# Performance work log

Hardware: AMD Instinct MI355X
Metric: run time of the kernel (lower is better)

The kernel has to match this reference:

```python
import jax, jax.numpy as jnp
import numpy as np
from jax import lax

N = 32768; L = 3000; PER_GRAPH = 64; NUM_GRAPHS = N // PER_GRAPH
DEG = 16; E = N * DEG
HID = 128; OUT3 = 64; NCLS = 2
RED = (L - 100) // 20 + 1   # 146
F_IN = 32 * RED             # 4672
EPS = 1e-5


def setup_inputs() -> dict:
    key = jax.random.key(0)
    ks = jax.random.split(key, 16)
    x = jax.random.normal(ks[0], (N, L), jnp.float32)
    # within-graph random edges: dst stays inside src's graph block
    src = jnp.repeat(jnp.arange(N, dtype=jnp.int32), DEG)
    dst = (src // PER_GRAPH) * PER_GRAPH + jax.random.randint(ks[1], (E,), 0, PER_GRAPH, dtype=jnp.int32)
    edge_index = jnp.stack([src, dst])
    edge_attr = jax.random.uniform(ks[2], (E,), jnp.float32, 0.1, 1.0)
    batch = jnp.repeat(jnp.arange(NUM_GRAPHS, dtype=jnp.int32), PER_GRAPH)
    g = lambda k, sh, fan: jax.random.normal(k, sh, jnp.float32) / np.float32(np.sqrt(fan))
    def bn(k, c):
        k1, k2 = jax.random.split(k)
        return (jnp.ones(c, jnp.float32), jnp.zeros(c, jnp.float32),
                0.1 * jax.random.normal(k1, (c,), jnp.float32),
                jax.random.uniform(k2, (c,), jnp.float32, 0.5, 1.5))
    g1, be1, m1, v1 = bn(ks[7], HID)
    g2, be2, m2, v2 = bn(ks[8], HID)
    g3, be3, m3, v3 = bn(ks[9], OUT3)
    return dict(x=x, edge_index=edge_index, edge_attr=edge_attr, batch=batch,
                conv_w=g(ks[3], (32, 1, 100), 100), conv_b=jnp.zeros(32, jnp.float32),
                W1=g(ks[4], (F_IN, HID), F_IN), b1=jnp.zeros(HID, jnp.float32),
                W2=g(ks[5], (HID, HID), HID), b2=jnp.zeros(HID, jnp.float32),
                W3=g(ks[6], (HID, OUT3), HID), b3=jnp.zeros(OUT3, jnp.float32),
                g1=g1, be1=be1, m1=m1, v1=v1,
                g2=g2, be2=be2, m2=m2, v2=v2,
                g3=g3, be3=be3, m3=m3, v3=v3,
                fc_w=g(ks[10], (OUT3, NCLS), OUT3), fc_b=jnp.zeros(NCLS, jnp.float32))


def _gcn(h, W, b, src, dst, w):
    # PyG GCNConv: linear (no bias) -> sym-normalized weighted aggregation with
    # self-loops (weight 1) -> + bias
    h = h @ W                                               # [N, C]
    deg = jax.ops.segment_sum(w, dst, num_segments=N) + 1.0  # + self-loop
    dinv = jnp.where(deg > 0, lax.rsqrt(deg), 0.0)
    norm = dinv[src] * w * dinv[dst]                         # [E]
    agg = jax.ops.segment_sum(h[src] * norm[:, None], dst, num_segments=N)
    return agg + h * (dinv * dinv)[:, None] + b              # self-loop term


def _bn(x, gamma, beta, mean, var):
    # eval-mode BatchNorm1d with running stats
    return (x - mean) * lax.rsqrt(var + EPS) * gamma + beta


def reference(x, edge_index, edge_attr, batch, conv_w, conv_b, W1, b1, W2, b2, W3, b3,
              g1, be1, m1, v1, g2, be2, m2, v2, g3, be3, m3, v3, fc_w, fc_b):
    src, dst = edge_index[0], edge_index[1]
    # Conv1d feature extractor: [N,1,L] -> [N,32,RED]
    h = lax.conv_general_dilated(x[:, None, :], conv_w, (20,), 'VALID',
                                 dimension_numbers=('NCH', 'OIH', 'NCH'))
    h = jax.nn.relu(h + conv_b[None, :, None]).reshape(N, F_IN)
    h = jax.nn.relu(_bn(_gcn(h, W1, b1, src, dst, edge_attr), g1, be1, m1, v1))
    h = jax.nn.relu(_bn(_gcn(h, W2, b2, src, dst, edge_attr), g2, be2, m2, v2))
    h = jax.nn.relu(_bn(_gcn(h, W3, b3, src, dst, edge_attr), g3, be3, m3, v3))
    # global mean pool over graphs
    sums = jax.ops.segment_sum(h, batch, num_segments=NUM_GRAPHS)
    cnt = jax.ops.segment_sum(jnp.ones((N,), h.dtype), batch, num_segments=NUM_GRAPHS)
    pooled = sums / cnt[:, None]
    return jax.nn.log_softmax(pooled @ fc_w + fc_b, axis=1)
```

## Files before the change

kernel.cpp:

```cpp
#include <hip/hip_runtime.h>
#include <math.h>

typedef float f32x4 __attribute__((ext_vector_type(4)));
typedef short bf16x8 __attribute__((ext_vector_type(8)));
typedef unsigned int u32;
typedef unsigned long long u64;

constexpr int N_NODES = 32768;
constexpr int LEN     = 3000;
constexpr int HID     = 128;
constexpr int OUT3    = 64;
constexpr int E_TOT   = 32768*16;
constexpr int PG      = 64;
constexpr int EPG     = 1024;
constexpr int NG      = 512;
constexpr int NCHUNK  = 25;
constexpr int XS_S    = 260;
constexpr int CBS     = 196;

__device__ __forceinline__ short bf1(float a) {
    unsigned u = __float_as_uint(a);
    return (short)((u + 0x7fff + ((u >> 16) & 1)) >> 16);
}
__device__ __forceinline__ u32 pk2(float lo, float hi) {
    u32 ua = __float_as_uint(lo) + 0x8000u;
    u32 ub = __float_as_uint(hi) + 0x8000u;
    return (ua >> 16) | (ub & 0xffff0000u);
}

__device__ __forceinline__ void bar_lds() {
    asm volatile("s_waitcnt lgkmcnt(0)" ::: "memory");
    __builtin_amdgcn_s_barrier();
}

__global__ void pack_w(const float* __restrict__ cw, short* __restrict__ wPf) {
    int tid = blockIdx.x * 256 + threadIdx.x;
    if (tid >= 512) return;
    int lane = tid & 63, i = tid >> 6;
    int Mt = i >> 2, ks = i & 3;
    int c  = Mt * 16 + (lane & 15);
    int kb = ks * 32 + (lane >> 4) * 8;
    bf16x8 v;
    #pragma unroll
    for (int j = 0; j < 8; j++) {
        int k = kb + j;
        v[j] = (k < 100) ? bf1(cw[c * 100 + k]) : (short)0;
    }
    *(bf16x8*)(wPf + tid * 8) = v;
}

__global__ void pack_w1(const float* __restrict__ W1, short* __restrict__ w1f) {
    int tid = blockIdx.x * 256 + threadIdx.x;
    if (tid >= 76800) return;
    int lane  = tid & 63;
    int rest  = tid >> 6;
    int ks    = rest % 6;
    int rest2 = rest / 6;
    int Nt    = rest2 & 7, chunk = rest2 >> 3;
    int r  = chunk * 6 + ks;
    int n  = Nt * 16 + (lane & 15);
    int cb = (lane >> 4) * 8;
    bf16x8 v;
    #pragma unroll
    for (int j = 0; j < 8; j++) {
        int c = cb + j;
        v[j] = (r < 146) ? bf1(W1[(c * 146 + r) * 128 + n]) : (short)0;
    }
    *(bf16x8*)(w1f + tid * 8) = v;
}

__global__ __launch_bounds__(256, 2) void conv_gemm1_mfma(
    const float* __restrict__ x, const short* __restrict__ wPf,
    const float* __restrict__ cbv, const short* __restrict__ w1f,
    float* __restrict__ z)
{
    __shared__ short xs[64 * XS_S];
    __shared__ short cbuf[64 * CBS];

    const int t     = threadIdx.x;
    const int lane  = t & 63;
    const int wv    = t >> 6;
    const int l15   = lane & 15;
    const int q     = lane >> 4;
    const int n0    = blockIdx.x * 64;
    const int j4    = lane & 3;
    const int nodeS = wv * 16 + (lane >> 2);
    const int nodeC = wv * 16 + l15;

    bf16x8 wA[8];
    #pragma unroll
    for (int i = 0; i < 8; i++)
        wA[i] = *(const bf16x8*)(wPf + (i * 64 + lane) * 8);
    float cbr[8];
    #pragma unroll
    for (int i = 0; i < 8; i++)
        cbr[i] = cbv[(i >> 2) * 16 + q * 4 + (i & 3)];

    f32x4 acc[4][2];
    #pragma unroll
    for (int a = 0; a < 4; a++) { acc[a][0] = (f32x4)0.0f; acc[a][1] = (f32x4)0.0f; }

    const int NtG0 = wv * 2;
    const float* xpS = x + (size_t)(n0 + nodeS) * LEN;
    short* xrow = xs + nodeS * XS_S;

    {
        float4 v[13];
        #pragma unroll
        for (int it = 0; it < 13; it++)
            v[it] = *(const float4*)(xpS + (j4 + 4 * it) * 4);
        #pragma unroll
        for (int it = 0; it < 13; it++) {
            int e = (j4 + 4 * it) * 4;
            *(uint2*)&xrow[e] = make_uint2(pk2(v[it].x, v[it].y), pk2(v[it].z, v[it].w));
        }
    }

    #pragma unroll 1
    for (int c = 0; c < NCHUNK; c++) {
        const int r0 = c * 6;
        const int rcount = (146 - r0 < 6) ? (146 - r0) : 6;

        float4 xn[8];
        if (c < NCHUNK - 1) {
            const int ebase = 120 * c + 200;
            #pragma unroll
            for (int it = 0; it < 8; it++) {
                int e  = ebase + (j4 + 4 * it) * 4;
                int ge = e > 2996 ? 2996 : e;
                xn[it] = *(const float4*)(xpS + ge);
            }
        }
        bf16x8 wB[12];
        #pragma unroll
        for (int u = 0; u < 12; u++)
            wB[u] = *(const bf16x8*)(w1f + ((c * 48 + NtG0 * 6 + u) * 64 + lane) * 8);

        bar_lds();

        const short* xr = xs + nodeC * XS_S;
        #pragma unroll
        for (int rr = 0; rr < 6; rr++) {
            const int eb = 20 * (r0 + rr) + 8 * q;
            f32x4 ca0 = (f32x4)0.0f, ca1 = (f32x4)0.0f;
            #pragma unroll
            for (int ks = 0; ks < 4; ks++) {
                int e0 = eb + 32 * ks;
                bf16x8 bx;
                *(u64*)&bx       = *(const u64*)&xr[e0 & 255];
                *((u64*)&bx + 1) = *(const u64*)&xr[(e0 + 4) & 255];
                ca0 = __builtin_amdgcn_mfma_f32_16x16x32_bf16(wA[ks],     bx, ca0, 0, 0, 0);
                ca1 = __builtin_amdgcn_mfma_f32_16x16x32_bf16(wA[4 + ks], bx, ca1, 0, 0, 0);
            }
            short* cw_ = cbuf + nodeC * CBS + rr * 32 + q * 4;
            if (rr < rcount) {
                u32 p0 = pk2(fmaxf(ca0[0] + cbr[0], 0.f), fmaxf(ca0[1] + cbr[1], 0.f));
                u32 p1 = pk2(fmaxf(ca0[2] + cbr[2], 0.f), fmaxf(ca0[3] + cbr[3], 0.f));
                *(uint2*)cw_ = make_uint2(p0, p1);
                p0 = pk2(fmaxf(ca1[0] + cbr[4], 0.f), fmaxf(ca1[1] + cbr[5], 0.f));
                p1 = pk2(fmaxf(ca1[2] + cbr[6], 0.f), fmaxf(ca1[3] + cbr[7], 0.f));
                *(uint2*)(cw_ + 16) = make_uint2(p0, p1);
            } else {
                *(uint2*)cw_        = make_uint2(0u, 0u);
                *(uint2*)(cw_ + 16) = make_uint2(0u, 0u);
            }
        }

        if (c < NCHUNK - 1) {
            const int ebase = 120 * c + 200;
            #pragma unroll
            for (int it = 0; it < 8; it++) {
                int e = ebase + (j4 + 4 * it) * 4;
                *(uint2*)&xrow[e & 255] = make_uint2(pk2(xn[it].x, xn[it].y), pk2(xn[it].z, xn[it].w));
            }
        }

        bar_lds();

        #pragma unroll
        for (int ks = 0; ks < 6; ks++) {
            bf16x8 af[4];
            #pragma unroll
            for (int mt = 0; mt < 4; mt++) {
                const short* ap = cbuf + (mt * 16 + l15) * CBS + ks * 32 + q * 8;
                *(u64*)&af[mt]       = *(const u64*)ap;
                *((u64*)&af[mt] + 1) = *(const u64*)(ap + 4);
            }
            #pragma unroll
            for (int mt = 0; mt < 4; mt++) {
                acc[mt][0] = __builtin_amdgcn_mfma_f32_16x16x32_bf16(af[mt], wB[ks],     acc[mt][0], 0, 0, 0);
                acc[mt][1] = __builtin_amdgcn_mfma_f32_16x16x32_bf16(af[mt], wB[6 + ks], acc[mt][1], 0, 0, 0);
            }
        }
    }

    #pragma unroll
    for (int mt = 0; mt < 4; mt++)
        #pragma unroll
        for (int nt2 = 0; nt2 < 2; nt2++)
            #pragma unroll
            for (int reg = 0; reg < 4; reg++) {
                int node = n0 + mt * 16 + q * 4 + reg;
                int f    = (NtG0 + nt2) * 16 + l15;
                z[(size_t)node * HID + f] = acc[mt][nt2][reg];
            }
}

__global__ __launch_bounds__(256) void graph_block(
    const float* __restrict__ z, const int* __restrict__ ei,
    const float* __restrict__ ew,
    const float* __restrict__ b1, const float* __restrict__ g1, const float* __restrict__ be1,
    const float* __restrict__ m1, const float* __restrict__ v1,
    const float* __restrict__ W2,
    const float* __restrict__ b2, const float* __restrict__ g2, const float* __restrict__ be2,
    const float* __restrict__ m2, const float* __restrict__ v2,
    const float* __restrict__ W3,
    const float* __restrict__ b3, const float* __restrict__ g3, const float* __restrict__ be3,
    const float* __restrict__ m3, const float* __restrict__ v3,
    const float* __restrict__ fcw, const float* __restrict__ fcb,
    float* __restrict__ out)
{
    __shared__ float At[64 * 68];
    __shared__ float buf[8704];
    __shared__ float dl[64];
    __shared__ float ps4[256];
    __shared__ float pooled[64];

    const int t  = threadIdx.x;
    const int g  = blockIdx.x;
    const int nb = g * PG;

    for (int i = t; i < 64 * 68; i += 256) At[i] = 0.f;
    if (t < 64) dl[t] = 0.f;
    __syncthreads();
    for (int i = t; i < EPG; i += 256) {
        int e = g * EPG + i;
        atomicAdd(&dl[ei[E_TOT + e] - nb], ew[e]);
    }
    __syncthreads();
    if (t < 64) dl[t] = rsqrtf(dl[t] + 1.0f);
    __syncthreads();
    for (int i = t; i < EPG; i += 256) {
        int e = g * EPG + i;
        int s = ei[e] - nb, d = ei[E_TOT + e] - nb;
        atomicAdd(&At[s * 68 + d], dl[s] * ew[e] * dl[d]);
    }
    if (t < 64) atomicAdd(&At[t * 68 + t], dl[t] * dl[t]);
    for (int i = t; i < 64 * HID; i += 256) buf[i] = z[(size_t)nb * HID + i];
    __syncthreads();

    const int f   = t & 127;
    const int ng  = t >> 7;
    const int n0  = ng * 32;
    const int f3  = t & 63;
    const int ng3 = t >> 6;
    const int n03 = ng3 * 16;

    float hreg[32];

#define LAYER128(BB, GG, BE, MM, VV)                                          \
    {                                                                         \
        float sc = GG[f] * rsqrtf(VV[f] + 1e-5f);                             \
        float mu = MM[f], bt = BE[f], bb = BB[f];                             \
        float a[32];                                                          \
        _Pragma("unroll")                                                     \
        for (int i = 0; i < 32; i++) a[i] = 0.f;                              \
        _Pragma("unroll 2")                                                   \
        for (int s = 0; s < 64; s++) {                                        \
            float zv = buf[s * 128 + f];                                      \
            _Pragma("unroll")                                                 \
            for (int qq = 0; qq < 8; qq++) {                                  \
                float4 a4 = *(const float4*)&At[s * 68 + n0 + qq * 4];        \
                a[qq*4+0] += a4.x * zv; a[qq*4+1] += a4.y * zv;               \
                a[qq*4+2] += a4.z * zv; a[qq*4+3] += a4.w * zv;               \
            }                                                                 \
        }                                                                     \
        _Pragma("unroll")                                                     \
        for (int i = 0; i < 32; i++)                                          \
            hreg[i] = fmaxf((a[i] + bb - mu) * sc + bt, 0.f);                 \
    }                                                                         \
    __syncthreads();                                                          \
    _Pragma("unroll")                                                         \
    for (int qq = 0; qq < 8; qq++)                                            \
        *(float4*)&buf[f * 68 + n0 + qq * 4] =                                \
            make_float4(hreg[qq*4], hreg[qq*4+1], hreg[qq*4+2], hreg[qq*4+3]);\
    __syncthreads();

#define GEMM128(WPTR)                                                         \
    {                                                                         \
        float a[32];                                                          \
        _Pragma("unroll")                                                     \
        for (int i = 0; i < 32; i++) a[i] = 0.f;                              \
        _Pragma("unroll 2")                                                   \
        for (int k = 0; k < 128; k++) {                                       \
            float wvv = WPTR[k * 128 + f];                                    \
            _Pragma("unroll")                                                 \
            for (int qq = 0; qq < 8; qq++) {                                  \
                float4 h4 = *(const float4*)&buf[k * 68 + n0 + qq * 4];       \
                a[qq*4+0] += h4.x * wvv; a[qq*4+1] += h4.y * wvv;             \
                a[qq*4+2] += h4.z * wvv; a[qq*4+3] += h4.w * wvv;             \
            }                                                                 \
        }                                                                     \
        __syncthreads();                                                      \
        _Pragma("unroll")                                                     \
        for (int i = 0; i < 32; i++) buf[(n0 + i) * 128 + f] = a[i];          \
        __syncthreads();                                                      \
    }

    LAYER128(b1, g1, be1, m1, v1)
    GEMM128(W2)
    LAYER128(b2, g2, be2, m2, v2)

    {
        float a[16];
        #pragma unroll
        for (int i = 0; i < 16; i++) a[i] = 0.f;
        #pragma unroll 2
        for (int k = 0; k < 128; k++) {
            float wvv = W3[k * 64 + f3];
            #pragma unroll
            for (int qq = 0; qq < 4; qq++) {
                float4 h4 = *(const float4*)&buf[k * 68 + n03 + qq * 4];
                a[qq*4+0] += h4.x * wvv; a[qq*4+1] += h4.y * wvv;
                a[qq*4+2] += h4.z * wvv; a[qq*4+3] += h4.w * wvv;
            }
        }
        __syncthreads();
        #pragma unroll
        for (int i = 0; i < 16; i++) buf[(n03 + i) * 64 + f3] = a[i];
        __syncthreads();
    }

    {
        float sc = g3[f3] * rsqrtf(v3[f3] + 1e-5f);
        float mu = m3[f3], bt = be3[f3], bb = b3[f3];
        float a[16];
        #pragma unroll
        for (int i = 0; i < 16; i++) a[i] = 0.f;
        #pragma unroll 2
        for (int s = 0; s < 64; s++) {
            float zv = buf[s * 64 + f3];
            #pragma unroll
            for (int qq = 0; qq < 4; qq++) {
                float4 a4 = *(const float4*)&At[s * 68 + n03 + qq * 4];
                a[qq*4+0] += a4.x * zv; a[qq*4+1] += a4.y * zv;
                a[qq*4+2] += a4.z * zv; a[qq*4+3] += a4.w * zv;
            }
        }
        float psum = 0.f;
        #pragma unroll
        for (int i = 0; i < 16; i++)
            psum += fmaxf((a[i] + bb - mu) * sc + bt, 0.f);
        ps4[ng3 * 64 + f3] = psum;
    }
    __syncthreads();
    if (t < 64) pooled[t] = (ps4[t] + ps4[64 + t] + ps4[128 + t] + ps4[192 + t]) * (1.f / 64.f);
    __syncthreads();
    if (t == 0) {
        float l0 = fcb[0], l1 = fcb[1];
        for (int ff = 0; ff < 64; ff++) { l0 += pooled[ff] * fcw[ff * 2]; l1 += pooled[ff] * fcw[ff * 2 + 1]; }
        float mx  = fmaxf(l0, l1);
        float lse = mx + logf(expf(l0 - mx) + expf(l1 - mx));
        out[g * 2 + 0] = l0 - lse;
        out[g * 2 + 1] = l1 - lse;
    }
#undef LAYER128
#undef GEMM128
}

extern "C" void kernel_launch(void* const* d_in, const int* in_sizes, int n_in,
                              void* d_out, int out_size, void* d_ws, size_t ws_size,
                              hipStream_t stream) {
    const float* x   = (const float*)d_in[0];
    const int*   ei  = (const int*)  d_in[1];
    const float* ew  = (const float*)d_in[2];
    const float* cw  = (const float*)d_in[4];
    const float* cb  = (const float*)d_in[5];
    const float* W1  = (const float*)d_in[6];
    const float* b1  = (const float*)d_in[7];
    const float* W2  = (const float*)d_in[8];
    const float* b2  = (const float*)d_in[9];
    const float* W3  = (const float*)d_in[10];
    const float* b3  = (const float*)d_in[11];
    const float* g1  = (const float*)d_in[12];
    const float* be1 = (const float*)d_in[13];
    const float* m1  = (const float*)d_in[14];
    const float* v1  = (const float*)d_in[15];
    const float* g2  = (const float*)d_in[16];
    const float* be2 = (const float*)d_in[17];
    const float* m2  = (const float*)d_in[18];
    const float* v2  = (const float*)d_in[19];
    const float* g3  = (const float*)d_in[20];
    const float* be3 = (const float*)d_in[21];
    const float* m3  = (const float*)d_in[22];
    const float* v3  = (const float*)d_in[23];
    const float* fcw = (const float*)d_in[24];
    const float* fcb = (const float*)d_in[25];
    float* out = (float*)d_out;

    float* z   = (float*)d_ws;
    short* wPf = (short*)((char*)d_ws + 16777216);
    short* w1f = (short*)((char*)d_ws + 16785408);

    pack_w  <<<2,   256, 0, stream>>>(cw, wPf);
    pack_w1 <<<300, 256, 0, stream>>>(W1, w1f);
    conv_gemm1_mfma<<<NG, 256, 0, stream>>>(x, wPf, cb, w1f, z);
    graph_block<<<NG, 256, 0, stream>>>(z, ei, ew,
        b1, g1, be1, m1, v1, W2,
        b2, g2, be2, m2, v2, W3,
        b3, g3, be3, m3, v3, fcw, fcb, out);
}
```

Measured before the change: 679.6 us.

## Fuse conv/GEMM1 kernel with per-graph GCN kernel via shared-memory handoff

Merges the conv+first-linear MFMA kernel and the per-graph GCN/BN/pool kernel into one kernel. Each block handles one graph and writes its z tile into shared memory instead of global memory. A single aliased shared buffer is reused across both phases. This removes the 16 MB z round trip and one launch, but the graph phase now runs under the (256,2) launch bound and the larger shared footprint, which may limit registers and occupancy.

```diff
diff --git a/kernel.cpp b/kernel.cpp
--- a/kernel.cpp
+++ b/kernel.cpp
@@ -69,20 +69,37 @@
     *(bf16x8*)(w1f + tid * 8) = v;
 }
 
-__global__ __launch_bounds__(256, 2) void conv_gemm1_mfma(
+__global__ __launch_bounds__(256, 2) void fused_all(
     const float* __restrict__ x, const short* __restrict__ wPf,
     const float* __restrict__ cbv, const short* __restrict__ w1f,
-    float* __restrict__ z)
+    const int* __restrict__ ei, const float* __restrict__ ew,
+    const float* __restrict__ b1, const float* __restrict__ g1, const float* __restrict__ be1,
+    const float* __restrict__ m1, const float* __restrict__ v1,
+    const float* __restrict__ W2,
+    const float* __restrict__ b2, const float* __restrict__ g2, const float* __restrict__ be2,
+    const float* __restrict__ m2, const float* __restrict__ v2,
+    const float* __restrict__ W3,
+    const float* __restrict__ b3, const float* __restrict__ g3, const float* __restrict__ be3,
+    const float* __restrict__ m3, const float* __restrict__ v3,
+    const float* __restrict__ fcw, const float* __restrict__ fcb,
+    float* __restrict__ out)
 {
-    __shared__ short xs[64 * XS_S];
-    __shared__ short cbuf[64 * CBS];
+    __shared__ __align__(16) char smraw[58368];
+    short* xs   = (short*)smraw;
+    short* cbuf = (short*)(smraw + 64 * XS_S * 2);
+    float* At     = (float*)smraw;
+    float* buf    = (float*)(smraw + 17408);
+    float* dl     = (float*)(smraw + 52224);
+    float* ps4    = (float*)(smraw + 52480);
+    float* pooled = (float*)(smraw + 53504);
 
     const int t     = threadIdx.x;
     const int lane  = t & 63;
     const int wv    = t >> 6;
     const int l15   = lane & 15;
     const int q     = lane >> 4;
-    const int n0    = blockIdx.x * 64;
+    const int g     = blockIdx.x;
+    const int nbase = g * 64;
     const int j4    = lane & 3;
     const int nodeS = wv * 16 + (lane >> 2);
     const int nodeC = wv * 16 + l15;
@@ -101,7 +118,7 @@
     for (int a = 0; a < 4; a++) { acc[a][0] = (f32x4)0.0f; acc[a][1] = (f32x4)0.0f; }
 
     const int NtG0 = wv * 2;
-    const float* xpS = x + (size_t)(n0 + nodeS) * LEN;
+    const float* xpS = x + (size_t)(nbase + nodeS) * LEN;
     short* xrow = xs + nodeS * XS_S;
 
     {
@@ -194,44 +211,22 @@
         }
     }
 
-    #pragma unroll
-    for (int mt = 0; mt < 4; mt++)
-        #pragma unroll
-        for (int nt2 = 0; nt2 < 2; nt2++)
-            #pragma unroll
-            for (int reg = 0; reg < 4; reg++) {
-                int node = n0 + mt * 16 + q * 4 + reg;
-                int f    = (NtG0 + nt2) * 16 + l15;
-                z[(size_t)node * HID + f] = acc[mt][nt2][reg];
-            }
-}
-
-__global__ __launch_bounds__(256) void graph_block(
-    const float* __restrict__ z, const int* __restrict__ ei,
-    const float* __restrict__ ew,
-    const float* __restrict__ b1, const float* __restrict__ g1, const float* __restrict__ be1,
-    const float* __restrict__ m1, const float* __restrict__ v1,
-    const float* __restrict__ W2,
-    const float* __restrict__ b2, const float* __restrict__ g2, const float* __restrict__ be2,
-    const float* __restrict__ m2, const float* __restrict__ v2,
-    const float* __restrict__ W3,
-    const float* __restrict__ b3, const float* __restrict__ g3, const float* __restrict__ be3,
-    const float* __restrict__ m3, const float* __restrict__ v3,
-    const float* __restrict__ fcw, const float* __restrict__ fcb,
-    float* __restrict__ out)
-{
-    __shared__ float At[64 * 68];
-    __shared__ float buf[8704];
-    __shared__ float dl[64];
-    __shared__ float ps4[256];
-    __shared__ float pooled[64];
-
-    const int t  = threadIdx.x;
-    const int g  = blockIdx.x;
-    const int nb = g * PG;
+    __syncthreads();
+
+    const int nb = nbase;
 
     for (int i = t; i < 64 * 68; i += 256) At[i] = 0.f;
     if (t < 64) dl[t] = 0.f;
+    #pragma unroll
+    for (int mt = 0; mt < 4; mt++)
+        #pragma unroll
+        for (int nt2 = 0; nt2 < 2; nt2++)
+            #pragma unroll
+            for (int reg = 0; reg < 4; reg++) {
+                int node = mt * 16 + q * 4 + reg;
+                int f    = (NtG0 + nt2) * 16 + l15;
+                buf[node * 128 + f] = acc[mt][nt2][reg];
+            }
     __syncthreads();
     for (int i = t; i < EPG; i += 256) {
         int e = g * EPG + i;
@@ -246,7 +241,6 @@
         atomicAdd(&At[s * 68 + d], dl[s] * ew[e] * dl[d]);
     }
     if (t < 64) atomicAdd(&At[t * 68 + t], dl[t] * dl[t]);
-    for (int i = t; i < 64 * HID; i += 256) buf[i] = z[(size_t)nb * HID + i];
     __syncthreads();
 
     const int f   = t & 127;
@@ -398,14 +392,12 @@
     const float* fcb = (const float*)d_in[25];
     float* out = (float*)d_out;
 
-    float* z   = (float*)d_ws;
     short* wPf = (short*)((char*)d_ws + 16777216);
     short* w1f = (short*)((char*)d_ws + 16785408);
 
     pack_w  <<<2,   256, 0, stream>>>(cw, wPf);
     pack_w1 <<<300, 256, 0, stream>>>(W1, w1f);
-    conv_gemm1_mfma<<<NG, 256, 0, stream>>>(x, wPf, cb, w1f, z);
-    graph_block<<<NG, 256, 0, stream>>>(z, ei, ew,
+    fused_all<<<NG, 256, 0, stream>>>(x, wPf, cb, w1f, ei, ew,
         b1, g1, be1, m1, v1, W2,
         b2, g2, be2, m2, v2, W3,
         b3, g3, be3, m3, v3, fcw, fcb, out);
```

Result: no change. 671.5 us (-1.2%).
